# Kernel tuning notes

Measured on AMD Instinct MI355X. Metric: run time of the kernel, lower is better.

The kernel has to match this reference:

```python
import jax, jax.numpy as jnp
import numpy as np

NUM_ITERS = 3

def squash(s, axis=-1):
    # standard capsule squash: ||s||^2/(1+||s||^2) * s/||s||
    sq = jnp.sum(s * s, axis=axis, keepdims=True)
    norm = jnp.sqrt(sq)
    return (sq / (1.0 + sq)) * (s / norm)

def setup_inputs() -> dict:
    key = jax.random.key(0)
    kx, kw = jax.random.split(key)
    B, I, k, l, O = 512, 1152, 8, 16, 7
    x = jax.random.normal(kx, (B, I, k), dtype=jnp.float32)
    w = jax.random.normal(kw, (I, k, l, O), dtype=jnp.float32)
    return {"x": x, "w": w}

def reference(x, w):
    # x: [B, I, k]; w: [I, k, l, O]
    u_hat = jnp.einsum('BIk,IklO->BIlO', x, w)            # [B, I, l, O]
    I, _, l, _ = w.shape
    b_ij = jnp.zeros((I, l), dtype=u_hat.dtype)
    v_j = None
    for _ in range(NUM_ITERS):
        c_ij = jax.nn.softmax(b_ij, axis=0)               # softmax over I
        s_j = jnp.einsum('Il,BIlO->BlO', c_ij, u_hat)     # [B, l, O]
        v_j = jnp.transpose(squash(s_j), (0, 2, 1))       # [B, O, l]
        u_vj = jnp.einsum('BOl,BIlO->BIl', v_j, u_hat).mean(axis=0)  # [I, l]
        b_ij = b_ij + u_vj
    return v_j
```

## Files before the change

kernel.cpp:

```cpp
#include <hip/hip_runtime.h>
#include <hip/hip_bf16.h>


#define NB 512
#define NI 1152
#define NLO 112
#define NIK 9216
#define NPAD 128

typedef __attribute__((ext_vector_type(8))) short bf16x8;
typedef __attribute__((ext_vector_type(4))) float f32x4;

__device__ __forceinline__ ushort f2bf(float f) {
    __hip_bfloat16 h = __float2bfloat16(f);
    return *(ushort*)&h;
}
__device__ __forceinline__ float bf2f(short s) {
    union { unsigned int u; float f; } v;
    v.u = ((unsigned int)(unsigned short)s) << 16;
    return v.f;
}

__device__ __forceinline__ void st_wt32(uint* p, uint v) {
    __hip_atomic_store(p, v, __ATOMIC_RELAXED, __HIP_MEMORY_SCOPE_AGENT);
}
__device__ __forceinline__ void st_wt64(unsigned long long* p, unsigned long long v) {
    __hip_atomic_store(p, v, __ATOMIC_RELAXED, __HIP_MEMORY_SCOPE_AGENT);
}
__device__ __forceinline__ float ld_cohf(const float* p) {
    return __hip_atomic_load((float*)p, __ATOMIC_RELAXED, __HIP_MEMORY_SCOPE_AGENT);
}

__device__ __forceinline__ void gbar_fence(int* ctr, int target) {
    __syncthreads();
    if (threadIdx.x == 0) {
        __threadfence();
        __hip_atomic_fetch_add(ctr, 1, __ATOMIC_RELAXED, __HIP_MEMORY_SCOPE_AGENT);
        while (__hip_atomic_load(ctr, __ATOMIC_RELAXED, __HIP_MEMORY_SCOPE_AGENT) < target)
            __builtin_amdgcn_s_sleep(2);
        __threadfence();
    }
    __syncthreads();
    __builtin_amdgcn_sched_barrier(0);
}

__device__ __forceinline__ void gbar_fast(int* ctr, int target) {
    __syncthreads();
    if (threadIdx.x == 0) {
        asm volatile("s_waitcnt vmcnt(0)" ::: "memory");
        __hip_atomic_fetch_add(ctr, 1, __ATOMIC_RELAXED, __HIP_MEMORY_SCOPE_AGENT);
        while (__hip_atomic_load(ctr, __ATOMIC_RELAXED, __HIP_MEMORY_SCOPE_AGENT) < target)
            __builtin_amdgcn_s_sleep(2);
    }
    __syncthreads();
    __builtin_amdgcn_sched_barrier(0);
}

__global__ __launch_bounds__(512, 2) void route_all(
        const float* __restrict__ x, const float* __restrict__ w,
        float* __restrict__ out,
        ushort* __restrict__ xbf, ushort* __restrict__ xT,
        ushort* __restrict__ wpT,
        ushort* __restrict__ wps0, ushort* __restrict__ wps1,
        ushort* __restrict__ vT0, ushort* __restrict__ vT1,
        float* __restrict__ Zbuf, int* __restrict__ bar) {
    __shared__ ushort tileA[64][68];
    __shared__ ushort tileW[NPAD][66];
    __shared__ float sp[8][16][16];
    __shared__ float ss[16][16];
    __shared__ float facs[16][2];
    __shared__ float zi[2];
    __shared__ float bs[2][8][16];
    __shared__ float cs[128];
    __shared__ float bij_s[128];
    const int bid = blockIdx.x;
    const int t = threadIdx.x;
    const int wv = t >> 6, lane = t & 63;
    const int row = lane & 15, quad = lane >> 4;

    for (int job = bid; job < 1296; job += 256) {
        if (job < 1152) {
            int kg = job % 144, bg = job / 144;
            int k0 = kg * 64, b0 = bg * 64;
            for (int e = t; e < 1024; e += 512) {
                int r = e >> 4, c4 = (e & 15) * 4;
                float4 f = *(const float4*)&x[(size_t)(b0 + r) * NIK + k0 + c4];
                ushort4 u = { f2bf(f.x), f2bf(f.y), f2bf(f.z), f2bf(f.w) };
                *(ushort4*)&xbf[(size_t)(b0 + r) * NIK + k0 + c4] = u;
                tileA[r][c4] = u.x; tileA[r][c4 + 1] = u.y;
                tileA[r][c4 + 2] = u.z; tileA[r][c4 + 3] = u.w;
            }
            __syncthreads();
            for (int e = t; e < 1024; e += 512) {
                int kr = e >> 4, c4 = (e & 15) * 4;
                ushort4 u = { tileA[c4][kr], tileA[c4 + 1][kr],
                              tileA[c4 + 2][kr], tileA[c4 + 3][kr] };
                *(ushort4*)&xT[(size_t)(k0 + kr) * NB + b0 + c4] = u;
            }
            __syncthreads();
        } else {
            int wb = job - 1152;
            int ik0 = wb * 64;
            for (int e = t; e < 8192; e += 512) {
                int ikl = e >> 7, np = e & 127;
                int l = np >> 3, o = np & 7;
                float wf = (o < 7) ? w[(size_t)(ik0 + ikl) * NLO + l * 7 + o] : 0.f;
                tileW[np][ikl] = f2bf(wf);
            }
            __syncthreads();
            for (int e = t; e < 8192; e += 512) {
                int np = e >> 6, ikl = e & 63;
                wpT[(size_t)np * NIK + ik0 + ikl] = tileW[np][ikl];
            }
            __syncthreads();
        }
    }
    int barv = 256;
    gbar_fence(bar, barv);

    const int mt = bid & 31, ng = bid >> 5;
    const int b0 = mt * 16, n0 = ng * 16;
    const int k0 = wv * 1152;
    const ushort* ap = xbf + (size_t)(b0 + row) * NIK + k0 + quad * 8;

    for (int it = 0; it < 3; ++it) {
        if (t < 2) zi[t] = (it == 0) ? (1.0f / 1152.0f)
                                     : 1.0f / ld_cohf(&Zbuf[it * 64 + ng * 2 + t]);
        const ushort* bsrc = (it == 0) ? wpT : ((it == 1) ? wps0 : wps1);
        const ushort* bp = bsrc + (size_t)(n0 + row) * NIK + k0 + quad * 8;
        f32x4 acc = {0.f, 0.f, 0.f, 0.f};
        #pragma unroll 6
        for (int ks = 0; ks < 36; ++ks) {
            bf16x8 a = *(const bf16x8*)(ap + ks * 32);
            bf16x8 b = *(const bf16x8*)(bp + ks * 32);
            acc = __builtin_amdgcn_mfma_f32_16x16x32_bf16(a, b, acc, 0, 0, 0);
        }
        #pragma unroll
        for (int r = 0; r < 4; ++r) sp[wv][quad * 4 + r][row] = acc[r];
        __syncthreads();
        if (t < 256) {
            int m = t >> 4, n = t & 15;
            float sv = 0.f;
            #pragma unroll
            for (int w8 = 0; w8 < 8; ++w8) sv += sp[w8][m][n];
            ss[m][n] = sv * zi[n >> 3];
        }
        __syncthreads();
        if (t < 32) {
            int m = t >> 1, ll = t & 1;
            float sq = 0.f;
            #pragma unroll
            for (int o = 0; o < 8; ++o) { float e = ss[m][ll * 8 + o]; sq += e * e; }
            facs[m][ll] = sqrtf(sq) / (1.0f + sq);
        }
        __syncthreads();
        if (t < 256) {
            int m = t >> 4, n = t & 15;
            float vv = ss[m][n] * facs[m][n >> 3];
            sp[0][m][n] = vv;
            if (it == 2) {
                int o = n & 7, lg = ng * 2 + (n >> 3);
                if (o < 7) out[(size_t)(b0 + m) * NLO + o * 16 + lg] = vv;
            }
        }
        if (it == 2) break;
        __syncthreads();
        if (t < 128) {
            int n = t >> 3, mp = t & 7;
            int o = n & 7, lg = ng * 2 + (n >> 3);
            if (o < 7) {
                uint lo = f2bf(sp[0][2 * mp][n]);
                uint hi = f2bf(sp[0][2 * mp + 1][n]);
                ushort* vTw = (it == 0) ? vT0 : vT1;
                st_wt32((uint*)(vTw + (size_t)(o * 16 + lg) * NB + b0 + 2 * mp),
                        lo | (hi << 16));
            }
        }
        barv += 256;
        gbar_fast(bar, barv);

        if (bid < 144) {
            const ushort* vTr = (it == 0) ? vT0 : vT1;
            int half = wv & 1;
            int mtg = wv >> 1;
            int m0 = bid * 64 + mtg * 16;
            int kb0 = half * 256;
            const ushort* gap = xT + (size_t)(m0 + row) * NB + kb0 + quad * 8;
            const ushort* gbp = vTr + (size_t)row * NB + kb0 + quad * 8;
            f32x4 gacc[7];
            #pragma unroll
            for (int nt = 0; nt < 7; ++nt) gacc[nt] = (f32x4){0.f, 0.f, 0.f, 0.f};
            for (int ks = 0; ks < 8; ++ks) {
                bf16x8 a = *(const bf16x8*)(gap + ks * 32);
                #pragma unroll
                for (int nt = 0; nt < 7; ++nt) {
                    bf16x8 bfr = *(const bf16x8*)(gbp + (size_t)nt * 16 * NB + ks * 32);
                    gacc[nt] = __builtin_amdgcn_mfma_f32_16x16x32_bf16(a, bfr, gacc[nt], 0, 0, 0);
                }
            }
            float S = 0.f;
            #pragma unroll
            for (int r = 0; r < 4; ++r) {
                int ik = m0 + quad * 4 + r;
                const float* wr = w + (size_t)ik * NLO + row * 7;
                float p = 0.f;
                #pragma unroll
                for (int o = 0; o < 7; ++o) p += wr[o] * gacc[o][r];
                S += p;
            }
            float Sp = __shfl_down(S, 16);
            if ((quad & 1) == 0)
                bs[half][mtg * 2 + (quad >> 1)][row] = (S + Sp) * (1.0f / 512.0f);
            __syncthreads();
            if (t < 128) {
                float val = bs[0][t >> 4][t & 15] + bs[1][t >> 4][t & 15];
                if (it) val += bij_s[t];
                bij_s[t] = val;
                cs[t] = expf(val);
            }
            __syncthreads();
            if (t < 16) {
                float z = 0.f;
                #pragma unroll
                for (int j = 0; j < 8; ++j) z += cs[j * 16 + t];
                __hip_atomic_fetch_add(&Zbuf[(it + 1) * 64 + t], z,
                                       __ATOMIC_RELAXED, __HIP_MEMORY_SCOPE_AGENT);
            }
            ushort* wpsw = (it == 0) ? wps0 : wps1;
            int ik0 = bid * 64;
            for (int e = t; e < 2048; e += 512) {
                int np = e >> 4, i4 = (e & 15) * 4;
                float sc = cs[(i4 >> 3) * 16 + (np >> 3)];
                ushort4 wv4 = *(const ushort4*)&wpT[(size_t)np * NIK + ik0 + i4];
                union { ushort4 s; unsigned long long q; } u;
                u.s = (ushort4){ f2bf(bf2f((short)wv4.x) * sc), f2bf(bf2f((short)wv4.y) * sc),
                                 f2bf(bf2f((short)wv4.z) * sc), f2bf(bf2f((short)wv4.w) * sc) };
                st_wt64((unsigned long long*)&wpsw[(size_t)np * NIK + ik0 + i4], u.q);
            }
        }
        barv += 256;
        gbar_fast(bar, barv);
    }
}

extern "C" void kernel_launch(void* const* d_in, const int* in_sizes, int n_in,
                              void* d_out, int out_size, void* d_ws, size_t ws_size,
                              hipStream_t stream) {
    const float* x = (const float*)d_in[0];
    const float* w = (const float*)d_in[1];
    float* out = (float*)d_out;
    float* ws = (float*)d_ws;
    float*  Zbuf = ws;
    int*    bar  = (int*)(ws + 192);
    ushort* xbf  = (ushort*)((char*)d_ws + 1024);
    ushort* xT   = xbf + (size_t)NB * NIK;
    ushort* wpT  = xT + (size_t)NIK * NB;
    ushort* wps0 = wpT + (size_t)NPAD * NIK;
    ushort* wps1 = wps0 + (size_t)NPAD * NIK;
    ushort* vT0  = wps1 + (size_t)NPAD * NIK;
    ushort* vT1  = vT0 + (size_t)NLO * NB;
    hipMemsetAsync(ws, 0, 1024, stream);
    route_all<<<256, 512, 0, stream>>>(x, w, out, xbf, xT, wpT, wps0, wps1,
                                       vT0, vT1, Zbuf, bar);
}
```

Baseline: 207.1 us.

## Apply routing coefficients on the fly and double threads per block

Removes the pre-scaled weight copies (wps0/wps1). Instead, the exp(b_ij) values are written to a small global buffer, staged into shared memory, and multiplied into the bf16 weight fragments inside the MFMA loop. Blocks grow from 512 to 1024 threads, which halves the K range each wave covers and splits the agreement GEMM into four K quarters. This drops a global write/read pass over the scaled weights between barriers, at the cost of extra ALU conversions in the inner loop and lower occupancy per CU.

```diff
diff --git a/kernel.cpp b/kernel.cpp
--- a/kernel.cpp
+++ b/kernel.cpp
@@ -23,12 +23,6 @@
 
 __device__ __forceinline__ void st_wt32(uint* p, uint v) {
     __hip_atomic_store(p, v, __ATOMIC_RELAXED, __HIP_MEMORY_SCOPE_AGENT);
-}
-__device__ __forceinline__ void st_wt64(unsigned long long* p, unsigned long long v) {
-    __hip_atomic_store(p, v, __ATOMIC_RELAXED, __HIP_MEMORY_SCOPE_AGENT);
-}
-__device__ __forceinline__ float ld_cohf(const float* p) {
-    return __hip_atomic_load((float*)p, __ATOMIC_RELAXED, __HIP_MEMORY_SCOPE_AGENT);
 }
 
 __device__ __forceinline__ void gbar_fence(int* ctr, int target) {
@@ -56,21 +50,22 @@
     __builtin_amdgcn_sched_barrier(0);
 }
 
-__global__ __launch_bounds__(512, 2) void route_all(
+__global__ __launch_bounds__(1024) void route_all(
         const float* __restrict__ x, const float* __restrict__ w,
         float* __restrict__ out,
         ushort* __restrict__ xbf, ushort* __restrict__ xT,
         ushort* __restrict__ wpT,
-        ushort* __restrict__ wps0, ushort* __restrict__ wps1,
+        float* __restrict__ eb0, float* __restrict__ eb1,
         ushort* __restrict__ vT0, ushort* __restrict__ vT1,
         float* __restrict__ Zbuf, int* __restrict__ bar) {
     __shared__ ushort tileA[64][68];
     __shared__ ushort tileW[NPAD][66];
-    __shared__ float sp[8][16][16];
+    __shared__ float csl[NI * 2];
+    __shared__ float sp[16][16][16];
     __shared__ float ss[16][16];
     __shared__ float facs[16][2];
     __shared__ float zi[2];
-    __shared__ float bs[2][8][16];
+    __shared__ float bs[4][8][16];
     __shared__ float cs[128];
     __shared__ float bij_s[128];
     const int bid = blockIdx.x;
@@ -82,8 +77,8 @@
         if (job < 1152) {
             int kg = job % 144, bg = job / 144;
             int k0 = kg * 64, b0 = bg * 64;
-            for (int e = t; e < 1024; e += 512) {
-                int r = e >> 4, c4 = (e & 15) * 4;
+            if (t < 1024) {
+                int r = t >> 4, c4 = (t & 15) * 4;
                 float4 f = *(const float4*)&x[(size_t)(b0 + r) * NIK + k0 + c4];
                 ushort4 u = { f2bf(f.x), f2bf(f.y), f2bf(f.z), f2bf(f.w) };
                 *(ushort4*)&xbf[(size_t)(b0 + r) * NIK + k0 + c4] = u;
@@ -91,8 +86,8 @@
                 tileA[r][c4 + 2] = u.z; tileA[r][c4 + 3] = u.w;
             }
             __syncthreads();
-            for (int e = t; e < 1024; e += 512) {
-                int kr = e >> 4, c4 = (e & 15) * 4;
+            if (t < 1024) {
+                int kr = t >> 4, c4 = (t & 15) * 4;
                 ushort4 u = { tileA[c4][kr], tileA[c4 + 1][kr],
                               tileA[c4 + 2][kr], tileA[c4 + 3][kr] };
                 *(ushort4*)&xT[(size_t)(k0 + kr) * NB + b0 + c4] = u;
@@ -101,14 +96,14 @@
         } else {
             int wb = job - 1152;
             int ik0 = wb * 64;
-            for (int e = t; e < 8192; e += 512) {
+            for (int e = t; e < 8192; e += 1024) {
                 int ikl = e >> 7, np = e & 127;
                 int l = np >> 3, o = np & 7;
                 float wf = (o < 7) ? w[(size_t)(ik0 + ikl) * NLO + l * 7 + o] : 0.f;
                 tileW[np][ikl] = f2bf(wf);
             }
             __syncthreads();
-            for (int e = t; e < 8192; e += 512) {
+            for (int e = t; e < 8192; e += 1024) {
                 int np = e >> 6, ikl = e & 63;
                 wpT[(size_t)np * NIK + ik0 + ikl] = tileW[np][ikl];
             }
@@ -120,19 +115,32 @@
 
     const int mt = bid & 31, ng = bid >> 5;
     const int b0 = mt * 16, n0 = ng * 16;
-    const int k0 = wv * 1152;
+    const int k0 = wv * 576;
+    const int lsel = row >> 3;
+    const int i0 = (k0 >> 3) + quad;
     const ushort* ap = xbf + (size_t)(b0 + row) * NIK + k0 + quad * 8;
+    const ushort* bp = wpT + (size_t)(n0 + row) * NIK + k0 + quad * 8;
 
     for (int it = 0; it < 3; ++it) {
-        if (t < 2) zi[t] = (it == 0) ? (1.0f / 1152.0f)
-                                     : 1.0f / ld_cohf(&Zbuf[it * 64 + ng * 2 + t]);
-        const ushort* bsrc = (it == 0) ? wpT : ((it == 1) ? wps0 : wps1);
-        const ushort* bp = bsrc + (size_t)(n0 + row) * NIK + k0 + quad * 8;
+        if (it == 0) {
+            for (int e = t; e < NI * 2; e += 1024) csl[e] = 1.0f;
+            if (t < 2) zi[t] = 1.0f / 1152.0f;
+        } else {
+            const float* ebr = (it == 1) ? eb0 : eb1;
+            for (int e = t; e < NI * 2; e += 1024)
+                csl[e] = ebr[(size_t)(e >> 1) * 16 + ng * 2 + (e & 1)];
+            if (t < 2) zi[t] = 1.0f / Zbuf[it * 64 + ng * 2 + t];
+        }
+        __syncthreads();
         f32x4 acc = {0.f, 0.f, 0.f, 0.f};
         #pragma unroll 6
-        for (int ks = 0; ks < 36; ++ks) {
+        for (int ks = 0; ks < 18; ++ks) {
             bf16x8 a = *(const bf16x8*)(ap + ks * 32);
-            bf16x8 b = *(const bf16x8*)(bp + ks * 32);
+            bf16x8 wf = *(const bf16x8*)(bp + ks * 32);
+            float cv = csl[(i0 + ks * 4) * 2 + lsel];
+            bf16x8 b;
+            #pragma unroll
+            for (int j = 0; j < 8; ++j) b[j] = (short)f2bf(bf2f(wf[j]) * cv);
             acc = __builtin_amdgcn_mfma_f32_16x16x32_bf16(a, b, acc, 0, 0, 0);
         }
         #pragma unroll
@@ -142,7 +150,7 @@
             int m = t >> 4, n = t & 15;
             float sv = 0.f;
             #pragma unroll
-            for (int w8 = 0; w8 < 8; ++w8) sv += sp[w8][m][n];
+            for (int w8 = 0; w8 < 16; ++w8) sv += sp[w8][m][n];
             ss[m][n] = sv * zi[n >> 3];
         }
         __syncthreads();
@@ -181,16 +189,16 @@
 
         if (bid < 144) {
             const ushort* vTr = (it == 0) ? vT0 : vT1;
-            int half = wv & 1;
-            int mtg = wv >> 1;
+            int qt = wv & 3;
+            int mtg = wv >> 2;
             int m0 = bid * 64 + mtg * 16;
-            int kb0 = half * 256;
+            int kb0 = qt * 128;
             const ushort* gap = xT + (size_t)(m0 + row) * NB + kb0 + quad * 8;
             const ushort* gbp = vTr + (size_t)row * NB + kb0 + quad * 8;
             f32x4 gacc[7];
             #pragma unroll
             for (int nt = 0; nt < 7; ++nt) gacc[nt] = (f32x4){0.f, 0.f, 0.f, 0.f};
-            for (int ks = 0; ks < 8; ++ks) {
+            for (int ks = 0; ks < 4; ++ks) {
                 bf16x8 a = *(const bf16x8*)(gap + ks * 32);
                 #pragma unroll
                 for (int nt = 0; nt < 7; ++nt) {
@@ -210,13 +218,18 @@
             }
             float Sp = __shfl_down(S, 16);
             if ((quad & 1) == 0)
-                bs[half][mtg * 2 + (quad >> 1)][row] = (S + Sp) * (1.0f / 512.0f);
+                bs[qt][mtg * 2 + (quad >> 1)][row] = (S + Sp) * (1.0f / 512.0f);
             __syncthreads();
             if (t < 128) {
-                float val = bs[0][t >> 4][t & 15] + bs[1][t >> 4][t & 15];
+                float val = bs[0][t >> 4][t & 15] + bs[1][t >> 4][t & 15]
+                          + bs[2][t >> 4][t & 15] + bs[3][t >> 4][t & 15];
                 if (it) val += bij_s[t];
                 bij_s[t] = val;
-                cs[t] = expf(val);
+                float e = expf(val);
+                cs[t] = e;
+                int i = bid * 8 + (t >> 4);
+                float* ebw = (it == 0) ? eb0 : eb1;
+                st_wt32((uint*)&ebw[(size_t)i * 16 + (t & 15)], __float_as_uint(e));
             }
             __syncthreads();
             if (t < 16) {
@@ -225,17 +238,6 @@
                 for (int j = 0; j < 8; ++j) z += cs[j * 16 + t];
                 __hip_atomic_fetch_add(&Zbuf[(it + 1) * 64 + t], z,
                                        __ATOMIC_RELAXED, __HIP_MEMORY_SCOPE_AGENT);
-            }
-            ushort* wpsw = (it == 0) ? wps0 : wps1;
-            int ik0 = bid * 64;
-            for (int e = t; e < 2048; e += 512) {
-                int np = e >> 4, i4 = (e & 15) * 4;
-                float sc = cs[(i4 >> 3) * 16 + (np >> 3)];
-                ushort4 wv4 = *(const ushort4*)&wpT[(size_t)np * NIK + ik0 + i4];
-                union { ushort4 s; unsigned long long q; } u;
-                u.s = (ushort4){ f2bf(bf2f((short)wv4.x) * sc), f2bf(bf2f((short)wv4.y) * sc),
-                                 f2bf(bf2f((short)wv4.z) * sc), f2bf(bf2f((short)wv4.w) * sc) };
-                st_wt64((unsigned long long*)&wpsw[(size_t)np * NIK + ik0 + i4], u.q);
             }
         }
         barv += 256;
@@ -251,15 +253,15 @@
     float* out = (float*)d_out;
     float* ws = (float*)d_ws;
     float*  Zbuf = ws;
-    int*    bar  = (int*)(ws + 192);
-    ushort* xbf  = (ushort*)((char*)d_ws + 1024);
+    int*    bar  = (int*)((char*)d_ws + 768);
+    float*  eb0  = (float*)((char*)d_ws + 1024);
+    float*  eb1  = eb0 + (size_t)NI * 16;
+    ushort* xbf  = (ushort*)(eb1 + (size_t)NI * 16);
     ushort* xT   = xbf + (size_t)NB * NIK;
     ushort* wpT  = xT + (size_t)NIK * NB;
-    ushort* wps0 = wpT + (size_t)NPAD * NIK;
-    ushort* wps1 = wps0 + (size_t)NPAD * NIK;
-    ushort* vT0  = wps1 + (size_t)NPAD * NIK;
+    ushort* vT0  = wpT + (size_t)NPAD * NIK;
     ushort* vT1  = vT0 + (size_t)NLO * NB;
     hipMemsetAsync(ws, 0, 1024, stream);
-    route_all<<<256, 512, 0, stream>>>(x, w, out, xbf, xT, wpT, wps0, wps1,
-                                       vT0, vT1, Zbuf, bar);
-}
+    route_all<<<256, 1024, 0, stream>>>(x, w, out, xbf, xT, wpT, eb0, eb1,
+                                        vT0, vT1, Zbuf, bar);
+}
```

Result: no change. 207.4 us (+0.2%).
